# Optimization experiments

Measured on AMD Instinct MI355X. Metric: run time of the kernel, lower is better.

Reference implementation:

```python
import jax, jax.numpy as jnp
import numpy as np

BN_EPS = 1e-5


def setup_inputs() -> dict:
    key = jax.random.key(0)
    k1, k2, k3, k4, k5 = jax.random.split(key, 5)
    N, E, D = 100000, 1600000, 128
    x = jax.random.normal(k1, (N, D), dtype=jnp.float32)
    edge_index = jax.random.randint(k2, (2, E), 0, N, dtype=jnp.int64)
    # GCNConv linear weight (PyG stores as [out, in], applied as x @ W.T) + post-agg bias
    W = jax.random.normal(k3, (D, D), dtype=jnp.float32) * (1.0 / np.sqrt(D))
    b = jax.random.normal(k4, (D,), dtype=jnp.float32) * 0.01
    gamma = jnp.ones((D,), dtype=jnp.float32)
    beta = jnp.zeros((D,), dtype=jnp.float32)
    return {"x": x, "edge_index": edge_index, "W": W, "b": b, "gamma": gamma, "beta": beta}


def reference(x, edge_index, W, b, gamma, beta):
    N = x.shape[0]
    src, dst = edge_index[0], edge_index[1]
    # GCN symmetric normalization (no self loops): deg over dst with unit weights
    deg = jax.ops.segment_sum(jnp.ones(src.shape[0], dtype=x.dtype), dst, num_segments=N)
    dinv = jnp.where(deg > 0, jax.lax.rsqrt(jnp.maximum(deg, 1.0)), 0.0)
    norm = dinv[src] * dinv[dst]                      # [E]
    xw = x @ W.T                                      # [N, D] linear transform first (fewer FLOPs)
    msg = xw[src] * norm[:, None]                     # [E, D] gather + scale
    agg = jax.ops.segment_sum(msg, dst, num_segments=N) + b  # [N, D] scatter-add + bias
    # BatchNorm1d over nodes (training-mode batch stats, biased variance)
    mu = jnp.mean(agg, axis=0)
    var = jnp.mean(jnp.square(agg - mu), axis=0)
    h = (agg - mu) * jax.lax.rsqrt(var + BN_EPS) * gamma + beta
    h = jax.nn.relu(h)
    return h + x
```

## Files before the change

kernel.cpp:

```cpp
#include <hip/hip_runtime.h>
#include <hip/hip_bf16.h>

#define DD 128
#define BN_EPS 1e-5f
#define BINSHIFT 8
#define EPB 8192
#define CAP 6144

typedef __attribute__((ext_vector_type(8))) short bf16x8;
typedef __attribute__((ext_vector_type(4))) float f32x4;

static __device__ __forceinline__ size_t rowoff(int r) { return (size_t)r * DD; }

static __device__ __forceinline__ ushort f2bf(float f) {
  __hip_bfloat16 h = __float2bfloat16(f);
  return __builtin_bit_cast(ushort, h);
}
static __device__ __forceinline__ float bf_lo(unsigned u) { return __uint_as_float(u << 16); }
static __device__ __forceinline__ float bf_hi(unsigned u) { return __uint_as_float(u & 0xffff0000u); }

__global__ __launch_bounds__(256) void k_scatter_convw(const int* __restrict__ src,
                                                       const int* __restrict__ dst,
                                                       int* __restrict__ gcursor,
                                                       unsigned* __restrict__ stg,
                                                       const float* __restrict__ W,
                                                       ushort* __restrict__ Wb,
                                                       int E, int NB, int nchunk) {
  int t = threadIdx.x;
  if (blockIdx.x == (unsigned)nchunk) {
#pragma unroll
    for (int i = 0; i < 16; ++i) {
      int f = i * 256 + t;
      int row = f >> 5, c4 = f & 31;
      float4 w = reinterpret_cast<const float4*>(W)[f];
      ushort4 p = make_ushort4(f2bf(w.x), f2bf(w.y), f2bf(w.z), f2bf(w.w));
      int chunk = (c4 >> 1) ^ (row & 7);
      *reinterpret_cast<ushort4*>(reinterpret_cast<char*>(Wb) + row * 256 +
                                  chunk * 16 + (c4 & 1) * 8) = p;
    }
    return;
  }
  __shared__ int hist[1024];
  __shared__ int base[1024];
  long long e0 = (long long)blockIdx.x * EPB;
  int eend = (int)((e0 + EPB < E) ? e0 + EPB : E);
  for (int i = t; i < NB; i += 256) hist[i] = 0;
  __syncthreads();
  for (int i = (int)e0 + t; i < eend; i += 256) atomicAdd(&hist[dst[i] >> BINSHIFT], 1);
  __syncthreads();
  for (int i = t; i < NB; i += 256) {
    int c = hist[i];
    base[i] = c ? (i * CAP + atomicAdd(&gcursor[i], c)) : 0;
    hist[i] = 0;
  }
  __syncthreads();
  for (int i = (int)e0 + t; i < eend; i += 256) {
    int d = dst[i];
    int bin = d >> BINSHIFT;
    unsigned v = ((unsigned)(d & 255) << 24) | (unsigned)src[i];
    int p = atomicAdd(&hist[bin], 1);
    stg[base[bin] + p] = v;
  }
}

__global__ __launch_bounds__(256) void k_gemm_binsort(const float* __restrict__ x,
                                                      const ushort* __restrict__ Wb,
                                                      ushort* __restrict__ xwb,
                                                      const unsigned* __restrict__ stg,
                                                      const int* __restrict__ gcursor,
                                                      int* __restrict__ ssrc,
                                                      int* __restrict__ offs,
                                                      int* __restrict__ oend,
                                                      float* __restrict__ dinv,
                                                      int N, int gG) {
  __shared__ char pool[65536];
  int t = threadIdx.x;

  if ((int)blockIdx.x >= gG) {
    int* hist = (int*)pool;
    int* scanb = (int*)(pool + 1024);
    int b = blockIdx.x - gG;
    int beg = b * CAP;
    int end = beg + gcursor[b];
    int nloc = N - b * 256;
    if (nloc > 256) nloc = 256;
    hist[t] = 0;
    __syncthreads();
    for (int i = beg + t; i < end; i += 256) atomicAdd(&hist[stg[i] >> 24], 1);
    __syncthreads();
    int h = hist[t];
    scanb[t] = h;
    __syncthreads();
    for (int off = 1; off < 256; off <<= 1) {
      int u = (t >= off) ? scanb[t - off] : 0;
      __syncthreads();
      scanb[t] += u;
      __syncthreads();
    }
    int myexcl = scanb[t] - h;
    __syncthreads();
    scanb[t] = myexcl;
    hist[t] = 0;
    int node = b * 256 + t;
    if (t < nloc) {
      offs[node] = beg + myexcl;
      oend[node] = beg + myexcl + h;
      dinv[node] = h > 0 ? rsqrtf((float)h) : 0.f;
    }
    __syncthreads();
    for (int i = beg + t; i < end; i += 256) {
      unsigned v = stg[i];
      int loc = v >> 24;
      int p = atomicAdd(&hist[loc], 1);
      ssrc[beg + scanb[loc] + p] = (int)(v & 0xFFFFFFu);
    }
    return;
  }

  ushort* Abuf = (ushort*)pool;
  ushort* Bbuf = (ushort*)(pool + 32768);
  int brow = blockIdx.x * 128;
  int wid = t >> 6, lane = t & 63;

  {
    const char* gW = reinterpret_cast<const char*>(Wb);
    char* lB = pool + 32768;
#pragma unroll
    for (int i = 0; i < 8; ++i) {
      int off = i * 4096 + wid * 1024;
      __builtin_amdgcn_global_load_lds(
          (const __attribute__((address_space(1))) void*)(gW + off + lane * 16),
          (__attribute__((address_space(3))) void*)(lB + off), 16, 0, 0);
    }
  }
  for (int i = 0; i < 16; ++i) {
    int f = i * 256 + t;
    int row = f >> 5, c4 = f & 31;
    int grow = brow + row;
    float4 v = make_float4(0.f, 0.f, 0.f, 0.f);
    if (grow < N) v = reinterpret_cast<const float4*>(x)[(size_t)grow * 32 + c4];
    ushort4 p = make_ushort4(f2bf(v.x), f2bf(v.y), f2bf(v.z), f2bf(v.w));
    int chunk = (c4 >> 1) ^ (row & 7);
    *reinterpret_cast<ushort4*>(reinterpret_cast<char*>(Abuf) + row * 256 +
                                chunk * 16 + (c4 & 1) * 8) = p;
  }
  __syncthreads();

  int kgrp = lane >> 4;
  int r0 = wid * 32 + (lane & 15);
  int r1 = r0 + 16;
  f32x4 acc[2][8];
#pragma unroll
  for (int rt = 0; rt < 2; ++rt)
#pragma unroll
    for (int cf = 0; cf < 8; ++cf) acc[rt][cf] = (f32x4){0.f, 0.f, 0.f, 0.f};

  const char* Ab = reinterpret_cast<const char*>(Abuf);
  const char* Bb = reinterpret_cast<const char*>(Bbuf);
#pragma unroll
  for (int ks = 0; ks < 4; ++ks) {
    int c = ks * 4 + kgrp;
    bf16x8 a0 = *reinterpret_cast<const bf16x8*>(Ab + r0 * 256 + ((c ^ (r0 & 7)) * 16));
    bf16x8 a1 = *reinterpret_cast<const bf16x8*>(Ab + r1 * 256 + ((c ^ (r1 & 7)) * 16));
#pragma unroll
    for (int cf = 0; cf < 8; ++cf) {
      int bc = cf * 16 + (lane & 15);
      bf16x8 bv = *reinterpret_cast<const bf16x8*>(Bb + bc * 256 + ((c ^ (bc & 7)) * 16));
      acc[0][cf] = __builtin_amdgcn_mfma_f32_16x16x32_bf16(a0, bv, acc[0][cf], 0, 0, 0);
      acc[1][cf] = __builtin_amdgcn_mfma_f32_16x16x32_bf16(a1, bv, acc[1][cf], 0, 0, 0);
    }
  }

#pragma unroll
  for (int rt = 0; rt < 2; ++rt) {
#pragma unroll
    for (int j = 0; j < 4; ++j) {
      int gr = brow + wid * 32 + rt * 16 + (lane >> 4) * 4 + j;
      if (gr < N) {
        ushort* orow = xwb + (size_t)gr * DD + (lane & 15);
#pragma unroll
        for (int cf = 0; cf < 8; ++cf) orow[cf * 16] = f2bf(acc[rt][cf][j]);
      }
    }
  }
}

__global__ __launch_bounds__(256) void k_aggregate(const int* __restrict__ offs,
                                                   const int* __restrict__ oend,
                                                   const int* __restrict__ ssrc,
                                                   const float* __restrict__ dinv,
                                                   const float* __restrict__ bvec,
                                                   const ushort* __restrict__ xwb,
                                                   float* __restrict__ agg,
                                                   ushort* __restrict__ aggb,
                                                   float* __restrict__ stats, int N) {
  __shared__ float red[1024];
  int t = threadIdx.x;
  int wid = t >> 6, lane = t & 63;
  float bc0 = bvec[2 * lane], bc1 = bvec[2 * lane + 1];
  float s0 = 0.f, q0 = 0.f, s1 = 0.f, q1 = 0.f;
  const unsigned laneb = lane * 2;

  for (int d = blockIdx.x * 4 + wid; d < N; d += gridDim.x * 4) {
    int off = offs[d], end = oend[d];
    float a0 = 0.f, a1 = 0.f, b0 = 0.f, b1 = 0.f;
    float c0 = 0.f, c1 = 0.f, e0 = 0.f, e1 = 0.f;
    int j = off;
    for (; j + 8 <= end; j += 8) {
      int sA = ssrc[j],     sB = ssrc[j + 1], sC = ssrc[j + 2], sD = ssrc[j + 3];
      int sE = ssrc[j + 4], sF = ssrc[j + 5], sG = ssrc[j + 6], sH = ssrc[j + 7];
      float nA = dinv[sA], nB = dinv[sB], nC = dinv[sC], nD = dinv[sD];
      float nE = dinv[sE], nF = dinv[sF], nG = dinv[sG], nH = dinv[sH];
      unsigned v0 = *reinterpret_cast<const unsigned*>(xwb + (size_t)sA * DD + laneb);
      unsigned v1 = *reinterpret_cast<const unsigned*>(xwb + (size_t)sB * DD + laneb);
      unsigned v2 = *reinterpret_cast<const unsigned*>(xwb + (size_t)sC * DD + laneb);
      unsigned v3 = *reinterpret_cast<const unsigned*>(xwb + (size_t)sD * DD + laneb);
      unsigned v4 = *reinterpret_cast<const unsigned*>(xwb + (size_t)sE * DD + laneb);
      unsigned v5 = *reinterpret_cast<const unsigned*>(xwb + (size_t)sF * DD + laneb);
      unsigned v6 = *reinterpret_cast<const unsigned*>(xwb + (size_t)sG * DD + laneb);
      unsigned v7 = *reinterpret_cast<const unsigned*>(xwb + (size_t)sH * DD + laneb);
      a0 = fmaf(bf_lo(v0), nA, a0); a1 = fmaf(bf_hi(v0), nA, a1);
      b0 = fmaf(bf_lo(v1), nB, b0); b1 = fmaf(bf_hi(v1), nB, b1);
      c0 = fmaf(bf_lo(v2), nC, c0); c1 = fmaf(bf_hi(v2), nC, c1);
      e0 = fmaf(bf_lo(v3), nD, e0); e1 = fmaf(bf_hi(v3), nD, e1);
      a0 = fmaf(bf_lo(v4), nE, a0); a1 = fmaf(bf_hi(v4), nE, a1);
      b0 = fmaf(bf_lo(v5), nF, b0); b1 = fmaf(bf_hi(v5), nF, b1);
      c0 = fmaf(bf_lo(v6), nG, c0); c1 = fmaf(bf_hi(v6), nG, c1);
      e0 = fmaf(bf_lo(v7), nH, e0); e1 = fmaf(bf_hi(v7), nH, e1);
    }
    if (j + 4 <= end) {
      int sA = ssrc[j], sB = ssrc[j + 1], sC = ssrc[j + 2], sD = ssrc[j + 3];
      float nA = dinv[sA], nB = dinv[sB], nC = dinv[sC], nD = dinv[sD];
      unsigned v0 = *reinterpret_cast<const unsigned*>(xwb + (size_t)sA * DD + laneb);
      unsigned v1 = *reinterpret_cast<const unsigned*>(xwb + (size_t)sB * DD + laneb);
      unsigned v2 = *reinterpret_cast<const unsigned*>(xwb + (size_t)sC * DD + laneb);
      unsigned v3 = *reinterpret_cast<const unsigned*>(xwb + (size_t)sD * DD + laneb);
      a0 = fmaf(bf_lo(v0), nA, a0); a1 = fmaf(bf_hi(v0), nA, a1);
      b0 = fmaf(bf_lo(v1), nB, b0); b1 = fmaf(bf_hi(v1), nB, b1);
      c0 = fmaf(bf_lo(v2), nC, c0); c1 = fmaf(bf_hi(v2), nC, c1);
      e0 = fmaf(bf_lo(v3), nD, e0); e1 = fmaf(bf_hi(v3), nD, e1);
      j += 4;
    }
    for (; j < end; ++j) {
      int sA = ssrc[j];
      float nA = dinv[sA];
      unsigned v0 = *reinterpret_cast<const unsigned*>(xwb + (size_t)sA * DD + laneb);
      a0 = fmaf(bf_lo(v0), nA, a0); a1 = fmaf(bf_hi(v0), nA, a1);
    }
    float dd = dinv[d];
    float r0 = ((a0 + b0) + (c0 + e0)) * dd;
    float r1 = ((a1 + b1) + (c1 + e1)) * dd;
    if (aggb) {
      unsigned pk = (unsigned)f2bf(r0) | ((unsigned)f2bf(r1) << 16);
      reinterpret_cast<unsigned*>(aggb + rowoff(d))[lane] = pk;
    } else {
      reinterpret_cast<float2*>(agg + rowoff(d))[lane] = make_float2(r0, r1);
    }
    float t0 = r0 + bc0, t1 = r1 + bc1;
    s0 += t0; q0 += t0 * t0;
    s1 += t1; q1 += t1 * t1;
  }

  float4* rw = reinterpret_cast<float4*>(red);
  rw[wid * 64 + lane] = make_float4(s0, q0, s1, q1);
  __syncthreads();
  {
    float v = red[t] + red[256 + t] + red[512 + t] + red[768 + t];
    int ln = t >> 2, k = t & 3;
    int col = 2 * ln + (k >> 1);
    int rep = blockIdx.x & 7;
    atomicAdd(&stats[rep * 256 + (k & 1) * 128 + col], v);
  }
}

__global__ __launch_bounds__(256) void k_final(float* __restrict__ out,
                                               const ushort* __restrict__ aggb,
                                               const float* __restrict__ x,
                                               const float* __restrict__ b,
                                               const float* __restrict__ gamma,
                                               const float* __restrict__ beta,
                                               const float* __restrict__ stats,
                                               float invN, int N) {
  __shared__ float muS[DD], rsS[DD];
  int t = threadIdx.x;
  if (t < DD) {
    float s = 0.f, q = 0.f;
#pragma unroll
    for (int rep = 0; rep < 8; ++rep) {
      s += stats[rep * 256 + t];
      q += stats[rep * 256 + 128 + t];
    }
    float mu = s * invN;
    float var = q * invN - mu * mu;
    muS[t] = mu;
    rsS[t] = rsqrtf(var + BN_EPS);
  }
  __syncthreads();

  long long i = (long long)blockIdx.x * 256 + threadIdx.x;
  long long stride = (long long)gridDim.x * 256;
  long long total = (long long)N * (DD / 4);
  const float4* __restrict__ x4 = reinterpret_cast<const float4*>(x);
  float4* __restrict__ o4 = reinterpret_cast<float4*>(out);
  const float4* __restrict__ b4 = reinterpret_cast<const float4*>(b);
  const float4* __restrict__ g4 = reinterpret_cast<const float4*>(gamma);
  const float4* __restrict__ be4 = reinterpret_cast<const float4*>(beta);
  const float4* muL = reinterpret_cast<const float4*>(muS);
  const float4* rsL = reinterpret_cast<const float4*>(rsS);
  for (; i < total; i += stride) {
    int c4 = (int)(i & (DD / 4 - 1));
    float4 v;
    if (aggb) {
      uint2 av = reinterpret_cast<const uint2*>(aggb)[i];
      v = make_float4(bf_lo(av.x), bf_hi(av.x), bf_lo(av.y), bf_hi(av.y));
    } else {
      v = o4[i];
    }
    float4 xv = x4[i];
    float4 bb = b4[c4], gg = g4[c4], be = be4[c4], mm = muL[c4], rr = rsL[c4];
    float4 o;
    o.x = fmaxf((v.x + bb.x - mm.x) * rr.x * gg.x + be.x, 0.f) + xv.x;
    o.y = fmaxf((v.y + bb.y - mm.y) * rr.y * gg.y + be.y, 0.f) + xv.y;
    o.z = fmaxf((v.z + bb.z - mm.z) * rr.z * gg.z + be.z, 0.f) + xv.z;
    o.w = fmaxf((v.w + bb.w - mm.w) * rr.w * gg.w + be.w, 0.f) + xv.w;
    o4[i] = o;
  }
}

extern "C" void kernel_launch(void* const* d_in, const int* in_sizes, int n_in,
                              void* d_out, int out_size, void* d_ws, size_t ws_size,
                              hipStream_t stream) {
  const float* x = (const float*)d_in[0];
  const int* ei = (const int*)d_in[1];
  const float* W = (const float*)d_in[2];
  const float* b = (const float*)d_in[3];
  const float* gamma = (const float*)d_in[4];
  const float* beta = (const float*)d_in[5];
  int N = in_sizes[0] / DD;
  int E = in_sizes[1] / 2;
  float* out = (float*)d_out;
  const int* src = ei;
  const int* dst = ei + E;
  int NB = (N + 255) >> BINSHIFT;

  ushort* xwb = (ushort*)d_ws;
  ushort* Wb = xwb + (size_t)N * DD;
  unsigned* stg = (unsigned*)(Wb + DD * DD);
  int* ssrc = (int*)(stg + (size_t)NB * CAP);
  int* offs = ssrc + (size_t)NB * CAP;
  int* oend = offs + N;
  float* dinv = (float*)(oend + N);
  int* gcursor = (int*)(dinv + N);
  float* stats = (float*)(gcursor + 1024);
  ushort* aggb = (ushort*)(stats + 2048);

  size_t need_aggb = (size_t)((char*)(aggb + (size_t)N * DD) - (char*)d_ws);
  if (ws_size < need_aggb) aggb = nullptr;

  hipMemsetAsync(gcursor, 0, 1024 * sizeof(int) + 2048 * sizeof(float), stream);

  int nchunk = (E + EPB - 1) / EPB;
  k_scatter_convw<<<nchunk + 1, 256, 0, stream>>>(src, dst, gcursor, stg, W, Wb,
                                                  E, NB, nchunk);

  int gG = (N + 127) / 128;
  k_gemm_binsort<<<gG + NB, 256, 0, stream>>>(x, Wb, xwb, stg, gcursor, ssrc,
                                              offs, oend, dinv, N, gG);

  k_aggregate<<<2048, 256, 0, stream>>>(offs, oend, ssrc, dinv, b, xwb, out, aggb,
                                        stats, N);

  k_final<<<2048, 256, 0, stream>>>(out, aggb, x, b, gamma, beta, stats,
                                    1.0f / (float)N, N);
}
```

Baseline: 174.8 us.

## Pre-scale GEMM output by source dinv and split binsort into separate kernel

Splits the fused GEMM+binsort kernel into a separate binsort kernel followed by the GEMM, so that dinv is available when the GEMM writes its output. The GEMM epilogue multiplies each row by dinv[src] before the bf16 store, which removes the per-edge dinv gather and the FMAs from the aggregate loop (they become plain adds). The cost is an extra kernel launch and the loss of overlap between the binsort and the GEMM. Rounding also changes, since the scale is now applied before the bf16 conversion.

```diff
diff --git a/kernel.cpp b/kernel.cpp
--- a/kernel.cpp
+++ b/kernel.cpp
@@ -63,68 +63,66 @@
   }
 }
 
-__global__ __launch_bounds__(256) void k_gemm_binsort(const float* __restrict__ x,
-                                                      const ushort* __restrict__ Wb,
-                                                      ushort* __restrict__ xwb,
-                                                      const unsigned* __restrict__ stg,
-                                                      const int* __restrict__ gcursor,
-                                                      int* __restrict__ ssrc,
-                                                      int* __restrict__ offs,
-                                                      int* __restrict__ oend,
-                                                      float* __restrict__ dinv,
-                                                      int N, int gG) {
-  __shared__ char pool[65536];
-  int t = threadIdx.x;
-
-  if ((int)blockIdx.x >= gG) {
-    int* hist = (int*)pool;
-    int* scanb = (int*)(pool + 1024);
-    int b = blockIdx.x - gG;
-    int beg = b * CAP;
-    int end = beg + gcursor[b];
-    int nloc = N - b * 256;
-    if (nloc > 256) nloc = 256;
-    hist[t] = 0;
+__global__ __launch_bounds__(256) void k_binsort(const unsigned* __restrict__ stg,
+                                                 const int* __restrict__ gcursor,
+                                                 int* __restrict__ ssrc,
+                                                 int* __restrict__ offs,
+                                                 int* __restrict__ oend,
+                                                 float* __restrict__ dinv,
+                                                 int N) {
+  __shared__ int hist[256];
+  __shared__ int scanb[256];
+  int b = blockIdx.x;
+  int t = threadIdx.x;
+  int beg = b * CAP;
+  int end = beg + gcursor[b];
+  int nloc = N - b * 256;
+  if (nloc > 256) nloc = 256;
+  hist[t] = 0;
+  __syncthreads();
+  for (int i = beg + t; i < end; i += 256) atomicAdd(&hist[stg[i] >> 24], 1);
+  __syncthreads();
+  int h = hist[t];
+  scanb[t] = h;
+  __syncthreads();
+  for (int off = 1; off < 256; off <<= 1) {
+    int u = (t >= off) ? scanb[t - off] : 0;
     __syncthreads();
-    for (int i = beg + t; i < end; i += 256) atomicAdd(&hist[stg[i] >> 24], 1);
+    scanb[t] += u;
     __syncthreads();
-    int h = hist[t];
-    scanb[t] = h;
-    __syncthreads();
-    for (int off = 1; off < 256; off <<= 1) {
-      int u = (t >= off) ? scanb[t - off] : 0;
-      __syncthreads();
-      scanb[t] += u;
-      __syncthreads();
-    }
-    int myexcl = scanb[t] - h;
-    __syncthreads();
-    scanb[t] = myexcl;
-    hist[t] = 0;
-    int node = b * 256 + t;
-    if (t < nloc) {
-      offs[node] = beg + myexcl;
-      oend[node] = beg + myexcl + h;
-      dinv[node] = h > 0 ? rsqrtf((float)h) : 0.f;
-    }
-    __syncthreads();
-    for (int i = beg + t; i < end; i += 256) {
-      unsigned v = stg[i];
-      int loc = v >> 24;
-      int p = atomicAdd(&hist[loc], 1);
-      ssrc[beg + scanb[loc] + p] = (int)(v & 0xFFFFFFu);
-    }
-    return;
-  }
-
-  ushort* Abuf = (ushort*)pool;
-  ushort* Bbuf = (ushort*)(pool + 32768);
+  }
+  int myexcl = scanb[t] - h;
+  __syncthreads();
+  scanb[t] = myexcl;
+  hist[t] = 0;
+  int node = b * 256 + t;
+  if (t < nloc) {
+    offs[node] = beg + myexcl;
+    oend[node] = beg + myexcl + h;
+    dinv[node] = h > 0 ? rsqrtf((float)h) : 0.f;
+  }
+  __syncthreads();
+  for (int i = beg + t; i < end; i += 256) {
+    unsigned v = stg[i];
+    int loc = v >> 24;
+    int p = atomicAdd(&hist[loc], 1);
+    ssrc[beg + scanb[loc] + p] = (int)(v & 0xFFFFFFu);
+  }
+}
+
+__global__ __launch_bounds__(256) void k_gemm_mfma(const float* __restrict__ x,
+                                                   const ushort* __restrict__ Wb,
+                                                   const float* __restrict__ dinv,
+                                                   ushort* __restrict__ xwb, int N) {
+  __shared__ ushort Abuf[128 * 128];
+  __shared__ ushort Bbuf[128 * 128];
+  int t = threadIdx.x;
   int brow = blockIdx.x * 128;
   int wid = t >> 6, lane = t & 63;
 
   {
     const char* gW = reinterpret_cast<const char*>(Wb);
-    char* lB = pool + 32768;
+    char* lB = reinterpret_cast<char*>(Bbuf);
 #pragma unroll
     for (int i = 0; i < 8; ++i) {
       int off = i * 4096 + wid * 1024;
@@ -177,9 +175,10 @@
     for (int j = 0; j < 4; ++j) {
       int gr = brow + wid * 32 + rt * 16 + (lane >> 4) * 4 + j;
       if (gr < N) {
+        float sc = dinv[gr];
         ushort* orow = xwb + (size_t)gr * DD + (lane & 15);
 #pragma unroll
-        for (int cf = 0; cf < 8; ++cf) orow[cf * 16] = f2bf(acc[rt][cf][j]);
+        for (int cf = 0; cf < 8; ++cf) orow[cf * 16] = f2bf(acc[rt][cf][j] * sc);
       }
     }
   }
@@ -209,8 +208,6 @@
     for (; j + 8 <= end; j += 8) {
       int sA = ssrc[j],     sB = ssrc[j + 1], sC = ssrc[j + 2], sD = ssrc[j + 3];
       int sE = ssrc[j + 4], sF = ssrc[j + 5], sG = ssrc[j + 6], sH = ssrc[j + 7];
-      float nA = dinv[sA], nB = dinv[sB], nC = dinv[sC], nD = dinv[sD];
-      float nE = dinv[sE], nF = dinv[sF], nG = dinv[sG], nH = dinv[sH];
       unsigned v0 = *reinterpret_cast<const unsigned*>(xwb + (size_t)sA * DD + laneb);
       unsigned v1 = *reinterpret_cast<const unsigned*>(xwb + (size_t)sB * DD + laneb);
       unsigned v2 = *reinterpret_cast<const unsigned*>(xwb + (size_t)sC * DD + laneb);
@@ -219,33 +216,31 @@
       unsigned v5 = *reinterpret_cast<const unsigned*>(xwb + (size_t)sF * DD + laneb);
       unsigned v6 = *reinterpret_cast<const unsigned*>(xwb + (size_t)sG * DD + laneb);
       unsigned v7 = *reinterpret_cast<const unsigned*>(xwb + (size_t)sH * DD + laneb);
-      a0 = fmaf(bf_lo(v0), nA, a0); a1 = fmaf(bf_hi(v0), nA, a1);
-      b0 = fmaf(bf_lo(v1), nB, b0); b1 = fmaf(bf_hi(v1), nB, b1);
-      c0 = fmaf(bf_lo(v2), nC, c0); c1 = fmaf(bf_hi(v2), nC, c1);
-      e0 = fmaf(bf_lo(v3), nD, e0); e1 = fmaf(bf_hi(v3), nD, e1);
-      a0 = fmaf(bf_lo(v4), nE, a0); a1 = fmaf(bf_hi(v4), nE, a1);
-      b0 = fmaf(bf_lo(v5), nF, b0); b1 = fmaf(bf_hi(v5), nF, b1);
-      c0 = fmaf(bf_lo(v6), nG, c0); c1 = fmaf(bf_hi(v6), nG, c1);
-      e0 = fmaf(bf_lo(v7), nH, e0); e1 = fmaf(bf_hi(v7), nH, e1);
+      a0 += bf_lo(v0); a1 += bf_hi(v0);
+      b0 += bf_lo(v1); b1 += bf_hi(v1);
+      c0 += bf_lo(v2); c1 += bf_hi(v2);
+      e0 += bf_lo(v3); e1 += bf_hi(v3);
+      a0 += bf_lo(v4); a1 += bf_hi(v4);
+      b0 += bf_lo(v5); b1 += bf_hi(v5);
+      c0 += bf_lo(v6); c1 += bf_hi(v6);
+      e0 += bf_lo(v7); e1 += bf_hi(v7);
     }
     if (j + 4 <= end) {
       int sA = ssrc[j], sB = ssrc[j + 1], sC = ssrc[j + 2], sD = ssrc[j + 3];
-      float nA = dinv[sA], nB = dinv[sB], nC = dinv[sC], nD = dinv[sD];
       unsigned v0 = *reinterpret_cast<const unsigned*>(xwb + (size_t)sA * DD + laneb);
       unsigned v1 = *reinterpret_cast<const unsigned*>(xwb + (size_t)sB * DD + laneb);
       unsigned v2 = *reinterpret_cast<const unsigned*>(xwb + (size_t)sC * DD + laneb);
       unsigned v3 = *reinterpret_cast<const unsigned*>(xwb + (size_t)sD * DD + laneb);
-      a0 = fmaf(bf_lo(v0), nA, a0); a1 = fmaf(bf_hi(v0), nA, a1);
-      b0 = fmaf(bf_lo(v1), nB, b0); b1 = fmaf(bf_hi(v1), nB, b1);
-      c0 = fmaf(bf_lo(v2), nC, c0); c1 = fmaf(bf_hi(v2), nC, c1);
-      e0 = fmaf(bf_lo(v3), nD, e0); e1 = fmaf(bf_hi(v3), nD, e1);
+      a0 += bf_lo(v0); a1 += bf_hi(v0);
+      b0 += bf_lo(v1); b1 += bf_hi(v1);
+      c0 += bf_lo(v2); c1 += bf_hi(v2);
+      e0 += bf_lo(v3); e1 += bf_hi(v3);
       j += 4;
     }
     for (; j < end; ++j) {
       int sA = ssrc[j];
-      float nA = dinv[sA];
       unsigned v0 = *reinterpret_cast<const unsigned*>(xwb + (size_t)sA * DD + laneb);
-      a0 = fmaf(bf_lo(v0), nA, a0); a1 = fmaf(bf_hi(v0), nA, a1);
+      a0 += bf_lo(v0); a1 += bf_hi(v0);
     }
     float dd = dinv[d];
     float r0 = ((a0 + b0) + (c0 + e0)) * dd;
@@ -363,9 +358,10 @@
   k_scatter_convw<<<nchunk + 1, 256, 0, stream>>>(src, dst, gcursor, stg, W, Wb,
                                                   E, NB, nchunk);
 
+  k_binsort<<<NB, 256, 0, stream>>>(stg, gcursor, ssrc, offs, oend, dinv, N);
+
   int gG = (N + 127) / 128;
-  k_gemm_binsort<<<gG + NB, 256, 0, stream>>>(x, Wb, xwb, stg, gcursor, ssrc,
-                                              offs, oend, dinv, N, gG);
+  k_gemm_mfma<<<gG, 256, 0, stream>>>(x, Wb, dinv, xwb, N);
 
   k_aggregate<<<2048, 256, 0, stream>>>(offs, oend, ssrc, dinv, b, xwb, out, aggb,
                                         stats, N);
```

New measurement: 154.2 us. 11.8% less time.
